# Performance work log

Hardware: AMD Instinct MI355X
Metric: run time of the kernel (lower is better)

## Reference

```python
import jax, jax.numpy as jnp
import numpy as np

B = 4096
D = 128
TEMP = 0.5
EPS = 1e-8  # torch cosine_similarity norm clamp


def setup_inputs() -> dict:
    key = jax.random.key(0)
    k1, k2 = jax.random.split(key)
    zi = jax.random.normal(k1, (B, D), dtype=jnp.float32)
    zj = jax.random.normal(k2, (B, D), dtype=jnp.float32)
    return {"zi": zi, "zj": zj}


def reference(zi, zj):
    b = zi.shape[0]
    n2 = 2 * b
    z = jnp.concatenate([zi, zj], axis=0)                      # (2N, D)
    norm = jnp.maximum(jnp.linalg.norm(z, axis=-1, keepdims=True), EPS)
    zn = z / norm
    sim = zn @ zn.T                                            # (2N, 2N) cosine similarity
    # positives: torch.diag(sim, +B) and torch.diag(sim, -B)
    right = jnp.diagonal(sim, offset=b)                        # sim[i, i+B]
    left = jnp.diagonal(sim, offset=-b)                        # sim[i+B, i]
    pos = jnp.concatenate([left, right]) / TEMP                # (2N,)
    # logits row i = [pos_i] + all sims except self-diagonal and the positive,
    # so the softmax denominator set = all entries except the self-diagonal.
    logits = sim / TEMP
    neg_big = jnp.asarray(jnp.finfo(logits.dtype).min, logits.dtype)
    masked = jnp.where(jnp.eye(n2, dtype=bool), neg_big, logits)
    lse = jax.nn.logsumexp(masked, axis=1)                     # (2N,)
    # CrossEntropyLoss(reduction='sum') with label 0, then / 2N
    loss = jnp.sum(lse - pos) / n2
    return loss
```

## Files before the change

### kernel.cpp

```cpp
#include <hip/hip_runtime.h>
#include <hip/hip_bf16.h>


#define BB 4096
#define N2 8192
#define DD 128
#define CSPLIT 32
#define CW (N2 / CSPLIT)
#define TW 64
#define NRD (CW / TW)

#define SCALE 1.69864360f

#if __has_builtin(__builtin_amdgcn_exp2f)
#define EXP2F(x) __builtin_amdgcn_exp2f(x)
#else
#define EXP2F(x) __expf((x) * 0.6931471805599453f)
#endif

using bf16 = __hip_bfloat16;
typedef __attribute__((ext_vector_type(8))) short short8;
typedef __attribute__((ext_vector_type(4))) float float4v;

__global__ __launch_bounds__(256) void ntx_norm_kernel(
    const float* __restrict__ zi, const float* __restrict__ zj,
    bf16* __restrict__ zn, float* __restrict__ rowsum, float* __restrict__ pos) {
  const int wave = threadIdx.x >> 6;
  const int lane = threadIdx.x & 63;
  const int pair = blockIdx.x * 4 + wave;
  float2 v = ((const float2*)(zi + (size_t)pair * DD))[lane];
  float2 w = ((const float2*)(zj + (size_t)pair * DD))[lane];
  float s1 = v.x * v.x + v.y * v.y;
  float s2 = w.x * w.x + w.y * w.y;
  float s3 = v.x * w.x + v.y * w.y;
  #pragma unroll
  for (int o = 32; o > 0; o >>= 1) {
    s1 += __shfl_xor(s1, o);
    s2 += __shfl_xor(s2, o);
    s3 += __shfl_xor(s3, o);
  }
  float nv = fmaxf(sqrtf(s1), 1e-8f);
  float nw = fmaxf(sqrtf(s2), 1e-8f);
  float rv = SCALE / nv, rw = SCALE / nw;
  bf16 bx = __float2bfloat16(v.x * rv);
  bf16 by = __float2bfloat16(v.y * rv);
  bf16 cx = __float2bfloat16(w.x * rw);
  bf16 cy = __float2bfloat16(w.y * rw);
  __hip_bfloat162 h2; h2.x = bx; h2.y = by;
  __hip_bfloat162 g2; g2.x = cx; g2.y = cy;
  ((__hip_bfloat162*)(zn + (size_t)pair * DD))[lane] = h2;
  ((__hip_bfloat162*)(zn + (size_t)(pair + BB) * DD))[lane] = g2;
  float fx = __bfloat162float(bx), fy = __bfloat162float(by);
  float gx = __bfloat162float(cx), gy = __bfloat162float(cy);
  float sii = fx * fx + fy * fy;
  float sjj = gx * gx + gy * gy;
  #pragma unroll
  for (int o = 32; o > 0; o >>= 1) {
    sii += __shfl_xor(sii, o);
    sjj += __shfl_xor(sjj, o);
  }
  if (lane == 0) {
    float c = s3 / (nv * nw);
    rowsum[pair]      = -EXP2F(sii);
    rowsum[pair + BB] = -EXP2F(sjj);
    pos[pair]      = c;
    pos[pair + BB] = c;
  }
}

__global__ __launch_bounds__(256) void ntx_sim_kernel(
    const bf16* __restrict__ zn, float* __restrict__ rowsum) {
  const int tid  = threadIdx.x;
  const int wave = tid >> 6;
  const int lane = tid & 63;
  const int quad = lane >> 4;
  const int l15  = lane & 15;
  const char* zb  = (const char*)zn;
  const short* zs = (const short*)zn;

  __shared__ float4 lds[2][TW * 16];

  const int rowBase  = blockIdx.y * 256 + wave * 64;
  const int colBase0 = blockIdx.x * CW;

  const int g0 = tid >> 4;
  const int sw = ((tid & 15) ^ (g0 & 7)) << 4;
  const char* srcb = zb + (size_t)(colBase0 + g0) * 256 + sw;

  float4 p0 = *(const float4*)(srcb);
  float4 p1 = *(const float4*)(srcb + 4096);
  float4 p2 = *(const float4*)(srcb + 8192);
  float4 p3 = *(const float4*)(srcb + 12288);

  short8 a[4][4];
  #pragma unroll
  for (int t = 0; t < 4; t++) {
    const short* ap = zs + (size_t)(rowBase + t * 16 + l15) * DD + quad * 8;
    #pragma unroll
    for (int c = 0; c < 4; c++) a[t][c] = *(const short8*)(ap + c * 32);
  }

  float rs[4][4];
  #pragma unroll
  for (int t = 0; t < 4; t++)
    #pragma unroll
    for (int r = 0; r < 4; r++) rs[t][r] = 0.0f;

  lds[0][tid] = p0;
  lds[0][tid + 256] = p1;
  lds[0][tid + 512] = p2;
  lds[0][tid + 768] = p3;
  __syncthreads();

  int cur = 0;
  #pragma unroll 1
  for (int rd = 0; rd < NRD; rd++) {
    float4 t0, t1, t2, t3;
    const bool pf = (rd + 1 < NRD);
    if (pf) {
      const char* sb = srcb + (size_t)(rd + 1) * (TW * 256);
      t0 = *(const float4*)(sb);
      t1 = *(const float4*)(sb + 4096);
      t2 = *(const float4*)(sb + 8192);
      t3 = *(const float4*)(sb + 12288);
    }

    const char* lb = (const char*)&lds[cur][0];
    #pragma unroll
    for (int k = 0; k < 4; k++) {
      short8 b[4];
      #pragma unroll
      for (int c = 0; c < 4; c++) {
        const int off = k * 4096 + l15 * 256 +
                        ((((c * 4 + quad) ^ (l15 & 7))) << 4);
        b[c] = *(const short8*)(lb + off);
      }
      #pragma unroll
      for (int t = 0; t < 4; t++) {
        float4v acc = {0.f, 0.f, 0.f, 0.f};
        acc = __builtin_amdgcn_mfma_f32_16x16x32_bf16(a[t][0], b[0], acc, 0, 0, 0);
        acc = __builtin_amdgcn_mfma_f32_16x16x32_bf16(a[t][1], b[1], acc, 0, 0, 0);
        acc = __builtin_amdgcn_mfma_f32_16x16x32_bf16(a[t][2], b[2], acc, 0, 0, 0);
        acc = __builtin_amdgcn_mfma_f32_16x16x32_bf16(a[t][3], b[3], acc, 0, 0, 0);
        #pragma unroll
        for (int r = 0; r < 4; r++) rs[t][r] += EXP2F(acc[r]);
      }
    }

    if (pf) {
      lds[cur ^ 1][tid] = t0;
      lds[cur ^ 1][tid + 256] = t1;
      lds[cur ^ 1][tid + 512] = t2;
      lds[cur ^ 1][tid + 768] = t3;
      __syncthreads();
      cur ^= 1;
    }
  }

  #pragma unroll
  for (int t = 0; t < 4; t++) {
    #pragma unroll
    for (int r = 0; r < 4; r++) {
      float s = rs[t][r];
      s += __shfl_xor(s, 1);
      s += __shfl_xor(s, 2);
      s += __shfl_xor(s, 4);
      s += __shfl_xor(s, 8);
      if (l15 == 0)
        atomicAdd(&rowsum[rowBase + t * 16 + quad * 4 + r], s);
    }
  }
}

__global__ __launch_bounds__(1024) void ntx_finalize_kernel(
    const float* __restrict__ rowsum, const float* __restrict__ pos,
    float* __restrict__ out) {
  float s = 0.f;
  for (int i = threadIdx.x; i < N2; i += 1024)
    s += __logf(rowsum[i]) - 2.0f * pos[i];
  #pragma unroll
  for (int o = 32; o > 0; o >>= 1) s += __shfl_xor(s, o);
  __shared__ float sm[16];
  const int wave = threadIdx.x >> 6;
  const int lane = threadIdx.x & 63;
  if (lane == 0) sm[wave] = s;
  __syncthreads();
  if (threadIdx.x == 0) {
    float t = 0.f;
    #pragma unroll
    for (int i = 0; i < 16; i++) t += sm[i];
    out[0] = t / (float)N2;
  }
}

extern "C" void kernel_launch(void* const* d_in, const int* in_sizes, int n_in,
                              void* d_out, int out_size, void* d_ws, size_t ws_size,
                              hipStream_t stream) {
  const float* zi = (const float*)d_in[0];
  const float* zj = (const float*)d_in[1];
  float* out = (float*)d_out;

  char* ws = (char*)d_ws;
  bf16* zn = (bf16*)ws;
  float* rowsum = (float*)(ws + (size_t)N2 * DD * 2);
  float* pos = rowsum + N2;

  ntx_norm_kernel<<<BB / 4, 256, 0, stream>>>(zi, zj, zn, rowsum, pos);
  dim3 grid(CSPLIT, N2 / 256);
  ntx_sim_kernel<<<grid, 256, 0, stream>>>(zn, rowsum);
  ntx_finalize_kernel<<<1, 1024, 0, stream>>>(rowsum, pos, out);
}
```

Before: 91.81 us.

## Fuse finalize reduction into sim kernel via last-block atomic counters

Removes the separate single-block finalize kernel. Each sim block bumps a per-row-panel counter, and the last block for a panel computes log(rowsum) minus the positive term for its 256 rows and atomically adds the result to a global accumulator. The last block overall writes the final loss. The counters are reset in the norm kernel. This saves a kernel launch and the serial 1024-thread pass, at the cost of extra fences and atomics. It also adds an occupancy hint to launch_bounds and makes the float summation order nondeterministic.

```diff
diff --git a/kernel.cpp b/kernel.cpp
--- a/kernel.cpp
+++ b/kernel.cpp
@@ -9,6 +9,8 @@
 #define CW (N2 / CSPLIT)
 #define TW 64
 #define NRD (CW / TW)
+#define NPANEL 32
+#define NBLOCKS (CSPLIT * NPANEL)
 
 #define SCALE 1.69864360f
 
@@ -24,9 +26,16 @@
 
 __global__ __launch_bounds__(256) void ntx_norm_kernel(
     const float* __restrict__ zi, const float* __restrict__ zj,
-    bf16* __restrict__ zn, float* __restrict__ rowsum, float* __restrict__ pos) {
+    bf16* __restrict__ zn, float* __restrict__ rowsum, float* __restrict__ pos,
+    float* __restrict__ accum, unsigned int* __restrict__ panelCnt,
+    unsigned int* __restrict__ globalCnt) {
   const int wave = threadIdx.x >> 6;
   const int lane = threadIdx.x & 63;
+  if (blockIdx.x == 0 && threadIdx.x < 34) {
+    if (threadIdx.x < 32) panelCnt[threadIdx.x] = 0u;
+    else if (threadIdx.x == 32) *globalCnt = 0u;
+    else *accum = 0.0f;
+  }
   const int pair = blockIdx.x * 4 + wave;
   float2 v = ((const float2*)(zi + (size_t)pair * DD))[lane];
   float2 w = ((const float2*)(zj + (size_t)pair * DD))[lane];
@@ -68,8 +77,11 @@
   }
 }
 
-__global__ __launch_bounds__(256) void ntx_sim_kernel(
-    const bf16* __restrict__ zn, float* __restrict__ rowsum) {
+__global__ __launch_bounds__(256, 4) void ntx_sim_kernel(
+    const bf16* __restrict__ zn, float* __restrict__ rowsum,
+    const float* __restrict__ pos, float* __restrict__ accum,
+    unsigned int* __restrict__ panelCnt, unsigned int* __restrict__ globalCnt,
+    float* __restrict__ out) {
   const int tid  = threadIdx.x;
   const int wave = tid >> 6;
   const int lane = tid & 63;
@@ -79,6 +91,8 @@
   const short* zs = (const short*)zn;
 
   __shared__ float4 lds[2][TW * 16];
+  __shared__ float psm[4];
+  __shared__ unsigned int lastPanel;
 
   const int rowBase  = blockIdx.y * 256 + wave * 64;
   const int colBase0 = blockIdx.x * CW;
@@ -170,26 +184,28 @@
         atomicAdd(&rowsum[rowBase + t * 16 + quad * 4 + r], s);
     }
   }
-}
-
-__global__ __launch_bounds__(1024) void ntx_finalize_kernel(
-    const float* __restrict__ rowsum, const float* __restrict__ pos,
-    float* __restrict__ out) {
-  float s = 0.f;
-  for (int i = threadIdx.x; i < N2; i += 1024)
-    s += __logf(rowsum[i]) - 2.0f * pos[i];
-  #pragma unroll
-  for (int o = 32; o > 0; o >>= 1) s += __shfl_xor(s, o);
-  __shared__ float sm[16];
-  const int wave = threadIdx.x >> 6;
-  const int lane = threadIdx.x & 63;
-  if (lane == 0) sm[wave] = s;
+
+  __threadfence();
+  if (tid == 0) lastPanel = atomicAdd(&panelCnt[blockIdx.y], 1u);
   __syncthreads();
-  if (threadIdx.x == 0) {
-    float t = 0.f;
-    #pragma unroll
-    for (int i = 0; i < 16; i++) t += sm[i];
-    out[0] = t / (float)N2;
+  if (lastPanel == CSPLIT - 1) {
+    const int r = blockIdx.y * 256 + tid;
+    float rsv  = atomicAdd(&rowsum[r], 0.0f);
+    float v = __logf(rsv) - 2.0f * pos[r];
+    #pragma unroll
+    for (int o = 32; o > 0; o >>= 1) v += __shfl_xor(v, o);
+    if (lane == 0) psm[wave] = v;
+    __syncthreads();
+    if (tid == 0) {
+      atomicAdd(accum, psm[0] + psm[1] + psm[2] + psm[3]);
+    }
+  }
+  __threadfence();
+  if (tid == 0) {
+    unsigned int g = atomicAdd(globalCnt, 1u);
+    if (g == NBLOCKS - 1) {
+      out[0] = atomicAdd(accum, 0.0f) / (float)N2;
+    }
   }
 }
 
@@ -204,9 +220,13 @@
   bf16* zn = (bf16*)ws;
   float* rowsum = (float*)(ws + (size_t)N2 * DD * 2);
   float* pos = rowsum + N2;
-
-  ntx_norm_kernel<<<BB / 4, 256, 0, stream>>>(zi, zj, zn, rowsum, pos);
-  dim3 grid(CSPLIT, N2 / 256);
-  ntx_sim_kernel<<<grid, 256, 0, stream>>>(zn, rowsum);
-  ntx_finalize_kernel<<<1, 1024, 0, stream>>>(rowsum, pos, out);
+  float* accum = pos + N2;
+  unsigned int* panelCnt = (unsigned int*)(accum + 1);
+  unsigned int* globalCnt = panelCnt + NPANEL;
+
+  ntx_norm_kernel<<<BB / 4, 256, 0, stream>>>(zi, zj, zn, rowsum, pos,
+                                              accum, panelCnt, globalCnt);
+  dim3 grid(CSPLIT, NPANEL);
+  ntx_sim_kernel<<<grid, 256, 0, stream>>>(zn, rowsum, pos, accum,
+                                           panelCnt, globalCnt, out);
 }
```

After: 346.0 us. 3.77x slower.

## Exploit similarity symmetry by computing only upper-triangular 128x128 tiles

Applied to the files above, without the earlier changes.

The similarity GEMM grid is reworked to cover only the upper-triangular panel pairs (I<=J) of 128x128 tiles. Each exp value is added to the row sums and also to per-column sums, which are reduced across waves in shared memory and atomically added to the column rows for off-diagonal tiles. This roughly halves the MFMA and exp work. In exchange it adds extra shuffles, an LDS column reduction, more atomics, and a smaller per-block tile with fewer A fragments per wave.

```diff
diff --git a/kernel.cpp b/kernel.cpp
--- a/kernel.cpp
+++ b/kernel.cpp
@@ -5,10 +5,13 @@
 #define BB 4096
 #define N2 8192
 #define DD 128
-#define CSPLIT 32
-#define CW (N2 / CSPLIT)
+#define NPAN 64
+#define PANROWS 128
+#define CW 128
 #define TW 64
-#define NRD (CW / TW)
+#define NRD 2
+#define NBLK2 (NPAN * (NPAN + 1) / 2)
+#define BUFBYTES (TW * 16 * 16)
 
 #define SCALE 1.69864360f
 
@@ -79,9 +82,15 @@
   const short* zs = (const short*)zn;
 
   __shared__ float4 lds[2][TW * 16];
-
-  const int rowBase  = blockIdx.y * 256 + wave * 64;
-  const int colBase0 = blockIdx.x * CW;
+  __shared__ float csum[4][CW];
+
+  int I = 0, rem = blockIdx.x;
+  while (rem >= NPAN - I) { rem -= NPAN - I; I++; }
+  const int J = I + rem;
+  const bool diag = (I == J);
+
+  const int rowBase  = I * PANROWS + wave * 32;
+  const int colBase0 = J * PANROWS;
 
   const int g0 = tid >> 4;
   const int sw = ((tid & 15) ^ (g0 & 7)) << 4;
@@ -92,17 +101,19 @@
   float4 p2 = *(const float4*)(srcb + 8192);
   float4 p3 = *(const float4*)(srcb + 12288);
 
-  short8 a[4][4];
-  #pragma unroll
-  for (int t = 0; t < 4; t++) {
+  short8 a[2][4];
+  #pragma unroll
+  for (int t = 0; t < 2; t++) {
     const short* ap = zs + (size_t)(rowBase + t * 16 + l15) * DD + quad * 8;
     #pragma unroll
     for (int c = 0; c < 4; c++) a[t][c] = *(const short8*)(ap + c * 32);
   }
-
-  float rs[4][4];
-  #pragma unroll
-  for (int t = 0; t < 4; t++)
+  asm volatile("" : "+v"(a[0][0]), "+v"(a[0][1]), "+v"(a[0][2]), "+v"(a[0][3]),
+                    "+v"(a[1][0]), "+v"(a[1][1]), "+v"(a[1][2]), "+v"(a[1][3]));
+
+  float rs[2][4];
+  #pragma unroll
+  for (int t = 0; t < 2; t++)
     #pragma unroll
     for (int r = 0; r < 4; r++) rs[t][r] = 0.0f;
 
@@ -112,6 +123,7 @@
   lds[0][tid + 768] = p3;
   __syncthreads();
 
+  char* ldsbase = (char*)&lds[0][0];
   int cur = 0;
   #pragma unroll 1
   for (int rd = 0; rd < NRD; rd++) {
@@ -125,7 +137,7 @@
       t3 = *(const float4*)(sb + 12288);
     }
 
-    const char* lb = (const char*)&lds[cur][0];
+    const char* lb = ldsbase + cur * BUFBYTES;
     #pragma unroll
     for (int k = 0; k < 4; k++) {
       short8 b[4];
@@ -135,16 +147,24 @@
                         ((((c * 4 + quad) ^ (l15 & 7))) << 4);
         b[c] = *(const short8*)(lb + off);
       }
+      float cvk = 0.0f;
       #pragma unroll
-      for (int t = 0; t < 4; t++) {
+      for (int t = 0; t < 2; t++) {
         float4v acc = {0.f, 0.f, 0.f, 0.f};
         acc = __builtin_amdgcn_mfma_f32_16x16x32_bf16(a[t][0], b[0], acc, 0, 0, 0);
         acc = __builtin_amdgcn_mfma_f32_16x16x32_bf16(a[t][1], b[1], acc, 0, 0, 0);
         acc = __builtin_amdgcn_mfma_f32_16x16x32_bf16(a[t][2], b[2], acc, 0, 0, 0);
         acc = __builtin_amdgcn_mfma_f32_16x16x32_bf16(a[t][3], b[3], acc, 0, 0, 0);
         #pragma unroll
-        for (int r = 0; r < 4; r++) rs[t][r] += EXP2F(acc[r]);
+        for (int r = 0; r < 4; r++) {
+          float e = EXP2F(acc[r]);
+          rs[t][r] += e;
+          cvk += e;
+        }
       }
+      cvk += __shfl_xor(cvk, 16);
+      cvk += __shfl_xor(cvk, 32);
+      if (quad == 0) csum[wave][rd * TW + k * 16 + l15] = cvk;
     }
 
     if (pf) {
@@ -158,7 +178,7 @@
   }
 
   #pragma unroll
-  for (int t = 0; t < 4; t++) {
+  for (int t = 0; t < 2; t++) {
     #pragma unroll
     for (int r = 0; r < 4; r++) {
       float s = rs[t][r];
@@ -170,6 +190,12 @@
         atomicAdd(&rowsum[rowBase + t * 16 + quad * 4 + r], s);
     }
   }
+
+  __syncthreads();
+  if (!diag && tid < CW) {
+    float s = csum[0][tid] + csum[1][tid] + csum[2][tid] + csum[3][tid];
+    atomicAdd(&rowsum[colBase0 + tid], s);
+  }
 }
 
 __global__ __launch_bounds__(1024) void ntx_finalize_kernel(
@@ -206,7 +232,6 @@
   float* pos = rowsum + N2;
 
   ntx_norm_kernel<<<BB / 4, 256, 0, stream>>>(zi, zj, zn, rowsum, pos);
-  dim3 grid(CSPLIT, N2 / 256);
-  ntx_sim_kernel<<<grid, 256, 0, stream>>>(zn, rowsum);
+  ntx_sim_kernel<<<NBLK2, 256, 0, stream>>>(zn, rowsum);
   ntx_finalize_kernel<<<1, 1024, 0, stream>>>(rowsum, pos, out);
 }
```

Measured after the change: 91.68 us. About the same (-0.1%).
